# Performance work log

Measured on AMD Instinct MI355X. Metric: run time of the kernel, lower is better.

The kernel has to match this reference:

```python
import jax, jax.numpy as jnp
from jax import lax
import numpy as np

ANCHOR_SCALES = [8, 16, 32]
ANCHOR_RATIOS = [0.5, 1.0, 2.0]
NUM_ANCHOR = len(ANCHOR_SCALES) * len(ANCHOR_RATIOS)
NMS_THRESH = 0.5


def _base_anchors(base_size=16):
    # generate_anchor_in_cell (called with defaults in the torch code)
    a = []
    for s in ANCHOR_SCALES:
        for r in ANCHOR_RATIOS:
            w = base_size * s * np.sqrt(r)
            h = w / r
            xmin = base_size / 2 - w / 2
            ymin = base_size / 2 - h / 2
            a.append([xmin, ymin, xmin + w, ymin + h])
    return np.array(a, dtype=np.float32)  # (A,4)


def _anchors_in_image(H, W, feature_stride):
    base = _base_anchors(16)  # torch code uses default stride for the base cell
    gx = np.arange(0, feature_stride * W, feature_stride)
    gy = np.arange(0, feature_stride * H, feature_stride)
    gx, gy = np.meshgrid(gx, gy)
    grid = np.stack([gx.ravel(), gy.ravel(), gx.ravel(), gy.ravel()], axis=1)  # (K,4)
    anc = (grid[:, None, :] + base[None, :, :]).reshape(-1, 4)  # (K*A,4)
    return jnp.asarray(anc, dtype=jnp.float32)


def _loc2bbox(anchors, loc):
    # anchors: (N,4) xyxy; loc: (B,N,4) (dx,dy,dw,dh)
    w = anchors[:, 2] - anchors[:, 0]
    h = anchors[:, 3] - anchors[:, 1]
    cx = anchors[:, 0] + 0.5 * w
    cy = anchors[:, 1] + 0.5 * h
    dx, dy, dw, dh = loc[..., 0], loc[..., 1], loc[..., 2], loc[..., 3]
    ncx = dx * w + cx
    ncy = dy * h + cy
    nw = jnp.exp(dw) * w
    nh = jnp.exp(dh) * h
    return jnp.stack([ncx - 0.5 * nw, ncy - 0.5 * nh,
                      ncx + 0.5 * nw, ncy + 0.5 * nh], axis=-1)


def _clip_bbox(rois, img_h, img_w):
    x = jnp.clip(rois[..., 0::2], 0.0, img_w)
    y = jnp.clip(rois[..., 1::2], 0.0, img_h)
    out = jnp.stack([x[..., 0], y[..., 0], x[..., 1], y[..., 1]], axis=-1)
    return out


def _nms(boxes, scores, thresh):
    # Greedy NMS. Returns (boxes_sorted_by_score, keep_mask) of fixed shape.
    N = boxes.shape[0]
    order = jnp.argsort(-scores)
    b = boxes[order]
    x1, y1, x2, y2 = b[:, 0], b[:, 1], b[:, 2], b[:, 3]
    areas = (x2 - x1) * (y2 - y1)
    idx = jnp.arange(N)

    def body(i, state):
        suppressed, keep = state
        cur = jnp.logical_not(suppressed[i])
        keep = keep.at[i].set(cur)
        bi = b[i]
        xx1 = jnp.maximum(bi[0], x1)
        yy1 = jnp.maximum(bi[1], y1)
        xx2 = jnp.minimum(bi[2], x2)
        yy2 = jnp.minimum(bi[3], y2)
        inter = jnp.maximum(xx2 - xx1, 0.0) * jnp.maximum(yy2 - yy1, 0.0)
        iou = inter / (areas[i] + areas - inter)
        sup = (iou > thresh) & cur & (idx > i)
        return (suppressed | sup, keep)

    suppressed0 = jnp.zeros((N,), dtype=bool)
    keep0 = jnp.zeros((N,), dtype=bool)
    _, keep = lax.fori_loop(0, N, body, (suppressed0, keep0))
    return b, keep, order


def reference(feature_map, feature_stride, conv_w, conv_b, score_w, score_b, loc_w, loc_b):
    B, C, H, W = feature_map.shape
    anchors = _anchors_in_image(H, W, feature_stride)  # (H*W*A, 4)

    dn = ('NCHW', 'OIHW', 'NCHW')
    mid = jax.nn.relu(lax.conv_general_dilated(
        feature_map, conv_w, (1, 1), ((1, 1), (1, 1)), dimension_numbers=dn)
        + conv_b[None, :, None, None])
    rpn_score = lax.conv_general_dilated(mid, score_w, (1, 1), ((0, 0), (0, 0)),
                                         dimension_numbers=dn) + score_b[None, :, None, None]
    rpn_loc = lax.conv_general_dilated(mid, loc_w, (1, 1), ((0, 0), (0, 0)),
                                       dimension_numbers=dn) + loc_b[None, :, None, None]

    # NCHW -> NHWC -> (B,H,W,A,2), softmax over the 2 classes
    rpn_score = jnp.transpose(rpn_score, (0, 2, 3, 1)).reshape(B, H, W, NUM_ANCHOR, 2)
    rpn_score = jax.nn.softmax(rpn_score, axis=4)
    rpn_loc = jnp.transpose(rpn_loc, (0, 2, 3, 1)).reshape(B, -1, 4)
    rpn_fg_score = rpn_score[..., 1].reshape(B, -1)
    rpn_score = rpn_score.reshape(B, -1, 2)

    rois = _loc2bbox(anchors, rpn_loc)                      # (B,N,4)
    rois = _clip_bbox(rois, H * feature_stride, W * feature_stride)

    # torch code flattens scores across batch -> effectively B == 1
    flat_rois = rois.reshape(-1, 4)
    flat_scores = rpn_fg_score.reshape(-1)
    b_sorted, keep, _ = _nms(lax.stop_gradient(flat_rois),
                             lax.stop_gradient(flat_scores), NMS_THRESH)
    # compacted kept rois (kept first, zero padding) at fixed shape
    order = jnp.argsort(-flat_scores)
    comp = jnp.argsort(~keep)  # stable: kept positions first
    rois_out = (flat_rois[order][comp] * keep[comp][:, None].astype(flat_rois.dtype))

    return rois_out, keep[comp], anchors, rpn_loc, rpn_score


def setup_inputs() -> dict:
    key = jax.random.key(0)
    k1, k2, k3, k4 = jax.random.split(key, 4)
    C_in, C_mid, A = 2048, 256, NUM_ANCHOR
    H, W = 38, 50
    feature_map = jax.random.normal(k1, (1, C_in, H, W), dtype=jnp.float32)
    conv_w = jax.random.normal(k2, (C_mid, C_in, 3, 3), dtype=jnp.float32) * 0.01
    conv_b = jnp.zeros((C_mid,), dtype=jnp.float32)
    score_w = jax.random.normal(k3, (A * 2, C_mid, 1, 1), dtype=jnp.float32) * 0.01
    score_b = jnp.zeros((A * 2,), dtype=jnp.float32)
    loc_w = jax.random.normal(k4, (A * 4, C_mid, 1, 1), dtype=jnp.float32) * 0.01
    loc_b = jnp.zeros((A * 4,), dtype=jnp.float32)
    return {"feature_map": feature_map, "feature_stride": 16,
            "conv_w": conv_w, "conv_b": conv_b,
            "score_w": score_w, "score_b": score_b,
            "loc_w": loc_w, "loc_b": loc_b}
```

## Files before the change

kernel.cpp:

```cpp
#include <hip/hip_runtime.h>
#include <cstdint>

#define U64 unsigned long long

static constexpr int H = 38, W = 50, P = 1900;
static constexpr int CIN = 2048, CMID = 256;
static constexpr int NA = 9, NBOX = 17100;
static constexpr int HP = 40, WP = 52, QP = HP * WP;
static constexpr int TPITCH = 2084;
static constexpr int KS = 7;
static constexpr int NW = 268;
static constexpr int PITCH = 17152;
static constexpr float NMS_T = 0.5f;
static constexpr int QTILE = 256;

static constexpr size_t SZ_INT  = (size_t)CIN * TPITCH * 4;
static constexpr size_t SZ_WT   = (size_t)9 * CIN * CMID * 4;
static constexpr size_t SZ_PART = (size_t)KS * P * CMID * 4;
static constexpr size_t OFF_INT  = 0;
static constexpr size_t OFF_WT   = OFF_INT + SZ_INT;
static constexpr size_t OFF_PART = OFF_WT + SZ_WT;
static constexpr size_t REGA     = OFF_PART + SZ_PART;
static constexpr size_t OFF_MASK = 0;
static constexpr size_t OFF_MID  = REGA;
static constexpr size_t OFF_FG   = OFF_MID + 1945600;
static constexpr size_t OFF_BOX  = OFF_FG + 68608;
static constexpr size_t OFF_SBOX = OFF_BOX + 273664;
static constexpr size_t OFF_SAREA= OFF_SBOX + 273664;
static constexpr size_t OFF_CNT  = OFF_SAREA + 68608;
static constexpr size_t WS_NEED  = OFF_CNT + 68608;

__device__ __forceinline__ U64 rdlane64(U64 v, int l) {
    unsigned lo = (unsigned)__builtin_amdgcn_readlane((int)(unsigned)(v & 0xffffffffull), l);
    unsigned hi = (unsigned)__builtin_amdgcn_readlane((int)(unsigned)(v >> 32), l);
    return ((U64)hi << 32) | (U64)lo;
}


__global__ __launch_bounds__(256) void k_sentinel(float* out, int n) {
    int i = blockIdx.x * 256 + threadIdx.x;
    if (i < n) out[i] = 1.2345678e8f;
}

__global__ __launch_bounds__(256) void k_in_t(const float* __restrict__ fm, float* __restrict__ in_tT) {
    int idx = blockIdx.x * 256 + threadIdx.x;
    if (idx >= CIN * (H * W)) return;
    int ci = idx / (H * W), hw = idx - ci * (H * W);
    int h = hw / W, w = hw - h * W;
    in_tT[(size_t)ci * TPITCH + (h + 1) * WP + 1 + w] = fm[idx];
}

__global__ __launch_bounds__(256) void k_w_t(const float* __restrict__ cw, float* __restrict__ w2) {
    int idx = blockIdx.x * 256 + threadIdx.x;
    if (idx >= CMID * CIN * 9) return;
    int co = idx / (CIN * 9);
    int rem = idx - co * (CIN * 9);
    int ci = rem / 9, k = rem - ci * 9;
    w2[((size_t)(co >> 3) * CIN + ci) * 72 + k * 8 + (co & 7)] = cw[idx];
}

__global__ __launch_bounds__(256, 2) void k_conv(const float* __restrict__ in_tT,
                                                 const float* __restrict__ w2,
                                                 float* __restrict__ partial) {
    __shared__ float4 s_in4[16 * 104];
    int t = threadIdx.x;
    int lane = t & 63;
    int sub = __builtin_amdgcn_readfirstlane(t >> 6);

    int raw = blockIdx.x;
    int xcd = raw & 7, i0 = raw >> 3;
    int L = xcd * 63 + i0;
    int z = L / 72;
    int r0 = L - z * 72;
    int bx = r0 % 9, by = r0 / 9;
    int q0 = bx * QTILE;
    int cout0 = by * 32;
    int cin0 = (z <= 1) ? 304 * z : 608 + 288 * (z - 2);
    int cin1 = cin0 + ((z <= 1) ? 304 : 288);

    float acc[4][8];
#pragma unroll
    for (int j = 0; j < 4; ++j)
#pragma unroll
        for (int c = 0; c < 8; ++c) acc[j][c] = 0.f;

    const float* wbase = w2 + (size_t)(by * 4 + sub) * CIN * 72;

    for (int c0 = cin0; c0 < cin1; c0 += 16) {
        for (int idx = t; idx < 16 * 92; idx += 256) {
            int r = idx / 92, j = idx - r * 92;
            int qf = q0 - 56 + 4 * j;
            float4 v = make_float4(0.f, 0.f, 0.f, 0.f);
            if (qf >= 0 && qf <= 2080)
                v = *reinterpret_cast<const float4*>(in_tT + (size_t)(c0 + r) * TPITCH + qf);
            s_in4[r * 104 + j + (j >> 3)] = v;
        }
        __syncthreads();
#pragma unroll 1
        for (int r = 0; r < 16; ++r) {
            const float4* row4 = s_in4 + r * 104;
            const float4* w4 = reinterpret_cast<const float4*>(wbase + (size_t)(c0 + r) * 72);
#pragma unroll
            for (int dy = 0; dy < 3; ++dy) {
                int v0 = lane + 13 * dy;
                int v1 = v0 + 1, v2 = v0 + 2;
                float4 F0 = row4[v0 + (v0 >> 3)];
                float4 F1 = row4[v1 + (v1 >> 3)];
                float4 F2 = row4[v2 + (v2 >> 3)];
                float F[12] = {F0.x, F0.y, F0.z, F0.w, F1.x, F1.y, F1.z, F1.w,
                               F2.x, F2.y, F2.z, F2.w};
#pragma unroll
                for (int dxi = 0; dxi < 3; ++dxi) {
                    int k = dy * 3 + dxi;
                    float4 wa = w4[k * 2], wb = w4[k * 2 + 1];
                    float wv[8] = {wa.x, wa.y, wa.z, wa.w, wb.x, wb.y, wb.z, wb.w};
#pragma unroll
                    for (int jj = 0; jj < 4; ++jj) {
                        float iv = F[jj + dxi + 3];
#pragma unroll
                        for (int c = 0; c < 8; ++c) acc[jj][c] += iv * wv[c];
                    }
                }
            }
        }
        __syncthreads();
    }
    float* part = partial + (size_t)z * P * CMID;
#pragma unroll
    for (int jj = 0; jj < 4; ++jj) {
        int q = q0 + 4 * lane + jj;
        if (q < QP) {
            int hp = q / WP, wp_ = q - hp * WP;
            if (hp >= 1 && hp <= H && wp_ >= 1 && wp_ <= W) {
                int p = (hp - 1) * W + (wp_ - 1);
                float* dst = part + (size_t)p * CMID + cout0 + sub * 8;
                float4* d4 = reinterpret_cast<float4*>(dst);
                d4[0] = make_float4(acc[jj][0], acc[jj][1], acc[jj][2], acc[jj][3]);
                d4[1] = make_float4(acc[jj][4], acc[jj][5], acc[jj][6], acc[jj][7]);
            }
        }
    }
}

__global__ __launch_bounds__(256) void k_reduce(const float* __restrict__ partial,
                                                const float* __restrict__ bias,
                                                float* __restrict__ mid) {
    int p = blockIdx.x, c = threadIdx.x;
    float s = bias[c];
    for (int ks = 0; ks < KS; ++ks) s += partial[(size_t)ks * P * CMID + (size_t)p * CMID + c];
    mid[(size_t)p * CMID + c] = fmaxf(s, 0.f);
}

__global__ __launch_bounds__(256) void k_heads(const float* __restrict__ mid,
                                               const float* __restrict__ score_w,
                                               const float* __restrict__ score_b,
                                               const float* __restrict__ loc_w,
                                               const float* __restrict__ loc_b,
                                               float* __restrict__ score_out,
                                               float* __restrict__ loc_out,
                                               float* __restrict__ anch_out,
                                               float* __restrict__ fg,
                                               float* __restrict__ boxes) {
    __shared__ float wl[256][56];
    __shared__ float bias[56];
    __shared__ float dots[4][64];
    int t = threadIdx.x;
    for (int idx = t; idx < 18 * 256; idx += 256) {
        int c = idx >> 8, i = idx & 255;
        wl[i][c] = score_w[idx];
    }
    for (int idx = t; idx < 36 * 256; idx += 256) {
        int c = idx >> 8, i = idx & 255;
        wl[i][18 + c] = loc_w[idx];
    }
    if (t < 18) bias[t] = score_b[t];
    else if (t < 54) bias[t] = loc_b[t - 18];
    __syncthreads();

    int pl = t >> 6, c = t & 63;
    for (int rep = 0; rep < 4; ++rep) {
        int p = blockIdx.x * 16 + rep * 4 + pl;
        if (c < 54 && p < P) {
            float d = bias[c];
            const float4* mp = reinterpret_cast<const float4*>(mid + (size_t)p * CMID);
            for (int i4 = 0; i4 < 64; ++i4) {
                float4 m4 = mp[i4];
                int i = i4 * 4;
                d += m4.x * wl[i][c] + m4.y * wl[i + 1][c] + m4.z * wl[i + 2][c] + m4.w * wl[i + 3][c];
            }
            dots[pl][c] = d;
        }
        __syncthreads();
        if (c < NA && p < P) {
            int a = c;
            int idx = p * NA + a;
            float l0 = dots[pl][2 * a], l1 = dots[pl][2 * a + 1];
            float mx = fmaxf(l0, l1);
            float e0 = expf(l0 - mx), e1 = expf(l1 - mx);
            float den = e0 + e1;
            float s0 = e0 / den, s1 = e1 / den;
            score_out[(size_t)idx * 2 + 0] = s0;
            score_out[(size_t)idx * 2 + 1] = s1;
            fg[idx] = s1;
            float dx = dots[pl][18 + 4 * a + 0];
            float dy = dots[pl][18 + 4 * a + 1];
            float dw = dots[pl][18 + 4 * a + 2];
            float dh = dots[pl][18 + 4 * a + 3];
            loc_out[(size_t)idx * 4 + 0] = dx;
            loc_out[(size_t)idx * 4 + 1] = dy;
            loc_out[(size_t)idx * 4 + 2] = dw;
            loc_out[(size_t)idx * 4 + 3] = dh;
            int hh = p / W, ww = p % W;
            const double scales[3] = {8.0, 16.0, 32.0};
            const double ratios[3] = {0.5, 1.0, 2.0};
            double s = scales[a / 3], r = ratios[a % 3];
            double wb2 = 16.0 * s * sqrt(r);
            double hb = wb2 / r;
            double xmin = 8.0 - wb2 / 2.0, ymin = 8.0 - hb / 2.0;
            float b0 = (float)xmin, b1 = (float)ymin;
            float b2 = (float)(xmin + wb2), b3 = (float)(ymin + hb);
            float gx = (float)(ww * 16), gy = (float)(hh * 16);
            float a0 = gx + b0, a1 = gy + b1, a2 = gx + b2, a3 = gy + b3;
            anch_out[(size_t)idx * 4 + 0] = a0;
            anch_out[(size_t)idx * 4 + 1] = a1;
            anch_out[(size_t)idx * 4 + 2] = a2;
            anch_out[(size_t)idx * 4 + 3] = a3;
            float aw = a2 - a0, ah = a3 - a1;
            float cx = a0 + 0.5f * aw, cy = a1 + 0.5f * ah;
            float ncx = dx * aw + cx, ncy = dy * ah + cy;
            float nw = expf(dw) * aw, nh = expf(dh) * ah;
            float x1 = ncx - 0.5f * nw, y1 = ncy - 0.5f * nh;
            float x2 = ncx + 0.5f * nw, y2 = ncy + 0.5f * nh;
            x1 = fminf(fmaxf(x1, 0.f), (float)(W * 16));
            x2 = fminf(fmaxf(x2, 0.f), (float)(W * 16));
            y1 = fminf(fmaxf(y1, 0.f), (float)(H * 16));
            y2 = fminf(fmaxf(y2, 0.f), (float)(H * 16));
            float4* bp = reinterpret_cast<float4*>(boxes);
            bp[idx] = make_float4(x1, y1, x2, y2);
        }
        __syncthreads();
    }
}

static constexpr int JSL = 2144;
__global__ __launch_bounds__(256) void k_rank_part(const float* __restrict__ fg,
                                                   int* __restrict__ cntb) {
    __shared__ float4 tile[256];
    int t = threadIdx.x;
    int i = blockIdx.x * 256 + t;
    int j0 = blockIdx.y * JSL;
    int j1 = min(NBOX, j0 + JSL);
    float my = (i < NBOX) ? fg[i] : 0.f;
    int cnt = 0;
    for (int base = j0; base < j1; base += 1024) {
        int j = base + t * 4;
        float4 v = make_float4(-3.4e38f, -3.4e38f, -3.4e38f, -3.4e38f);
        if (j + 3 < j1) {
            v = *reinterpret_cast<const float4*>(fg + j);
        } else {
            if (j < j1) v.x = fg[j];
            if (j + 1 < j1) v.y = fg[j + 1];
            if (j + 2 < j1) v.z = fg[j + 2];
            if (j + 3 < j1) v.w = fg[j + 3];
        }
        __syncthreads();
        tile[t] = v;
        __syncthreads();
        if (i < NBOX) {
            for (int u = 0; u < 256; ++u) {
                float4 s = tile[u];
                int jb = base + u * 4;
                cnt += (s.x > my) || (s.x == my && jb < i);
                cnt += (s.y > my) || (s.y == my && jb + 1 < i);
                cnt += (s.z > my) || (s.z == my && jb + 2 < i);
                cnt += (s.w > my) || (s.w == my && jb + 3 < i);
            }
        }
    }
    if (i < NBOX && cnt) atomicAdd(&cntb[i], cnt);
}

__global__ __launch_bounds__(256) void k_scatter(const int* __restrict__ cntb,
                                                 const float* __restrict__ boxes,
                                                 float* __restrict__ sboxes,
                                                 float* __restrict__ sarea) {
    int i = blockIdx.x * 256 + threadIdx.x;
    if (i >= NBOX) return;
    int c = cntb[i];
    float4 b = reinterpret_cast<const float4*>(boxes)[i];
    reinterpret_cast<float4*>(sboxes)[c] = b;
    sarea[c] = (b.z - b.x) * (b.w - b.y);
}

__global__ __launch_bounds__(256) void k_maskfill(const float* __restrict__ sboxes,
                                                  const float* __restrict__ sarea,
                                                  U64* __restrict__ maskT) {
    int w = blockIdx.y;
    int i0 = blockIdx.x * 256;
    if (w < (i0 >> 6)) return;
    __shared__ float4 sb[64];
    __shared__ float sa[64];
    int t = threadIdx.x;
    if (t < 64) {
        int j = w * 64 + t;
        if (j < NBOX) {
            sb[t] = reinterpret_cast<const float4*>(sboxes)[j];
            sa[t] = sarea[j];
        } else {
            sb[t] = make_float4(0.f, 0.f, 0.f, 0.f);
            sa[t] = 0.f;
        }
    }
    __syncthreads();
    int i = i0 + t;
    if (i >= NBOX || w < (i >> 6)) return;
    float4 bi = reinterpret_cast<const float4*>(sboxes)[i];
    float ai = sarea[i];
    U64 word = 0;
#pragma unroll 4
    for (int jb = 0; jb < 64; ++jb) {
        int j = w * 64 + jb;
        float4 bj = sb[jb];
        float xx1 = fmaxf(bi.x, bj.x), yy1 = fmaxf(bi.y, bj.y);
        float xx2 = fminf(bi.z, bj.z), yy2 = fminf(bi.w, bj.w);
        float inter = fmaxf(xx2 - xx1, 0.f) * fmaxf(yy2 - yy1, 0.f);
        float iou = inter / (ai + sa[jb] - inter);
        word |= ((U64)((iou > NMS_T) && (j > i))) << jb;
    }
    maskT[(size_t)w * PITCH + i] = word;
}

__global__ __launch_bounds__(256) void k_sweep(const U64* __restrict__ maskT,
                                               const float* __restrict__ sboxes,
                                               float* __restrict__ rois_out,
                                               float* __restrict__ keep_out) {
    __shared__ U64 rem[NW];
    __shared__ U64 diag[2][64];
    __shared__ int klist[64];
    __shared__ unsigned base_s;
    int t = threadIdx.x;
    for (int u = t; u < NW; u += 256) rem[u] = 0;
    if (t == 0) base_s = 0;
    if (t < 64) diag[0][t] = maskT[t];
    __syncthreads();

    for (int g = 0; g < NW; ++g) {
        int nv = min(64, NBOX - g * 64);
        U64 vmask = (nv == 64) ? ~0ull : ((1ull << nv) - 1);

        U64 nxtval = 0;
        if (t < 64 && g + 1 < NW) {
            int row = (g + 1) * 64 + t;
            if (row < NBOX) nxtval = maskT[(size_t)(g + 1) * PITCH + row];
        }

        U64 myw = diag[g & 1][t & 63];
        U64 notsup = ~rem[g] & vmask;
        U64 kept = 0;
        while (notsup) {
            int i = (int)__builtin_ctzll(notsup);
            kept |= (1ull << i);
            U64 wi = rdlane64(myw, i);
            notsup &= ~(wi | (1ull << i));
        }
        int nk = __popcll(kept);
        unsigned base = base_s;

        if (t < 64) {
            if ((kept >> t) & 1ull) {
                unsigned pre = (unsigned)__popcll(kept & ((1ull << t) - 1));
                unsigned dst = base + pre;
                float4 bb = reinterpret_cast<const float4*>(sboxes)[g * 64 + t];
                reinterpret_cast<float4*>(rois_out)[dst] = bb;
                keep_out[dst] = 1.0f;
                klist[pre] = t;
            }
        }
        __syncthreads();

        if (t == 0) base_s = base + (unsigned)nk;

        for (int w = g + 1 + t; w < NW; w += 256) {
            const U64* col = maskT + (size_t)w * PITCH + g * 64;
            U64 acc = rem[w];
            int b = 0;
            for (; b + 7 < nk; b += 8) {
                U64 v0 = col[klist[b]];
                U64 v1 = col[klist[b + 1]];
                U64 v2 = col[klist[b + 2]];
                U64 v3 = col[klist[b + 3]];
                U64 v4 = col[klist[b + 4]];
                U64 v5 = col[klist[b + 5]];
                U64 v6 = col[klist[b + 6]];
                U64 v7 = col[klist[b + 7]];
                acc |= v0 | v1 | v2 | v3 | v4 | v5 | v6 | v7;
            }
            for (; b + 3 < nk; b += 4) {
                U64 v0 = col[klist[b]];
                U64 v1 = col[klist[b + 1]];
                U64 v2 = col[klist[b + 2]];
                U64 v3 = col[klist[b + 3]];
                acc |= v0 | v1 | v2 | v3;
            }
            for (; b < nk; ++b) acc |= col[klist[b]];
            rem[w] = acc;
        }
        if (t < 64) diag[(g + 1) & 1][t] = nxtval;
        __syncthreads();
    }
}

extern "C" void kernel_launch(void* const* d_in, const int* in_sizes, int n_in,
                              void* d_out, int out_size, void* d_ws, size_t ws_size,
                              hipStream_t stream) {
    const float* fm      = (const float*)d_in[0];
    const float* conv_w  = (const float*)d_in[2];
    const float* conv_b  = (const float*)d_in[3];
    const float* score_w = (const float*)d_in[4];
    const float* score_b = (const float*)d_in[5];
    const float* loc_w   = (const float*)d_in[6];
    const float* loc_b   = (const float*)d_in[7];

    float* out = (float*)d_out;
    float* rois_out  = out;
    float* keep_out  = out + NBOX * 4;
    float* anch_out  = out + NBOX * 5;
    float* loc_out   = out + NBOX * 9;
    float* score_out = out + NBOX * 13;

    if (ws_size < WS_NEED) {
        k_sentinel<<<(out_size + 255) / 256, 256, 0, stream>>>(out, out_size);
        return;
    }

    char* ws = (char*)d_ws;
    float* in_tT   = (float*)(ws + OFF_INT);
    float* w2      = (float*)(ws + OFF_WT);
    float* partial = (float*)(ws + OFF_PART);
    U64*   maskT   = (U64*)(ws + OFF_MASK);
    float* mid     = (float*)(ws + OFF_MID);
    float* fg      = (float*)(ws + OFF_FG);
    float* boxes   = (float*)(ws + OFF_BOX);
    float* sboxes  = (float*)(ws + OFF_SBOX);
    float* sarea   = (float*)(ws + OFF_SAREA);
    int*   cntb    = (int*)(ws + OFF_CNT);

    hipMemsetAsync(in_tT, 0, SZ_INT, stream);
    k_in_t<<<(CIN * H * W + 255) / 256, 256, 0, stream>>>(fm, in_tT);
    k_w_t<<<(CMID * CIN * 9 + 255) / 256, 256, 0, stream>>>(conv_w, w2);
    k_conv<<<504, 256, 0, stream>>>(in_tT, w2, partial);
    k_reduce<<<P, 256, 0, stream>>>(partial, conv_b, mid);
    k_heads<<<(P + 15) / 16, 256, 0, stream>>>(mid, score_w, score_b, loc_w, loc_b,
                                               score_out, loc_out, anch_out, fg, boxes);
    hipMemsetAsync(cntb, 0, NBOX * 4, stream);
    k_rank_part<<<dim3((NBOX + 255) / 256, 8), 256, 0, stream>>>(fg, cntb);
    k_scatter<<<(NBOX + 255) / 256, 256, 0, stream>>>(cntb, boxes, sboxes, sarea);
    hipMemsetAsync(rois_out, 0, (size_t)NBOX * 5 * 4, stream);
    k_maskfill<<<dim3((NBOX + 255) / 256, NW), 256, 0, stream>>>(sboxes, sarea, maskT);
    k_sweep<<<1, 256, 0, stream>>>(maskT, sboxes, rois_out, keep_out);
}
```

Baseline: 867.9 us.

## Pipeline NMS sweep: wave0 resolves groups while other waves propagate previous suppression

Restructures the greedy NMS sweep so one wavefront resolves each 64-box group and directly ORs its kept rows into the next group's suppression mask using register-held prefetched words. The remaining three wavefronts propagate the previous group's suppression to later groups one step behind, using atomicOr on shared memory. This halves the block barriers per group and overlaps the serial scan with the column propagation. In exchange it relies on LDS atomics and lagged propagation, and it prefetches mask rows two groups ahead in registers.

New measurement: 852.5 us. No clear change (-1.8%).

```diff
diff --git a/kernel.cpp b/kernel.cpp
--- a/kernel.cpp
+++ b/kernel.cpp
@@ -335,78 +335,91 @@
                                                float* __restrict__ rois_out,
                                                float* __restrict__ keep_out) {
     __shared__ U64 rem[NW];
-    __shared__ U64 diag[2][64];
-    __shared__ int klist[64];
+    __shared__ int klbuf[2][64];
+    __shared__ int kn[2];
     __shared__ unsigned base_s;
     int t = threadIdx.x;
     for (int u = t; u < NW; u += 256) rem[u] = 0;
-    if (t == 0) base_s = 0;
-    if (t < 64) diag[0][t] = maskT[t];
+    if (t == 0) { base_s = 0; kn[0] = 0; kn[1] = 0; }
+
+    U64 dA = 0, nA = 0, dB = 0, nB = 0;
+    if (t < 64) {
+        int r0 = t;
+        dA = maskT[(size_t)0 * PITCH + r0];
+        nA = maskT[(size_t)1 * PITCH + r0];
+        int r1 = 64 + t;
+        dB = maskT[(size_t)1 * PITCH + r1];
+        nB = maskT[(size_t)2 * PITCH + r1];
+    }
     __syncthreads();
 
-    for (int g = 0; g < NW; ++g) {
-        int nv = min(64, NBOX - g * 64);
-        U64 vmask = (nv == 64) ? ~0ull : ((1ull << nv) - 1);
-
-        U64 nxtval = 0;
-        if (t < 64 && g + 1 < NW) {
-            int row = (g + 1) * 64 + t;
-            if (row < NBOX) nxtval = maskT[(size_t)(g + 1) * PITCH + row];
-        }
-
-        U64 myw = diag[g & 1][t & 63];
-        U64 notsup = ~rem[g] & vmask;
-        U64 kept = 0;
-        while (notsup) {
-            int i = (int)__builtin_ctzll(notsup);
-            kept |= (1ull << i);
-            U64 wi = rdlane64(myw, i);
-            notsup &= ~(wi | (1ull << i));
-        }
-        int nk = __popcll(kept);
-        unsigned base = base_s;
-
+    auto body = [&](int g, U64& dR, U64& nR) {
         if (t < 64) {
-            if ((kept >> t) & 1ull) {
+            int nv = min(64, NBOX - g * 64);
+            U64 vmask = (nv == 64) ? ~0ull : ((1ull << nv) - 1);
+            U64 m = rem[g];
+            U64 notsup = ~m & vmask;
+            U64 kept = 0;
+            while (notsup) {
+                int i = (int)__builtin_ctzll(notsup);
+                kept |= (1ull << i);
+                U64 wi = rdlane64(dR, i);
+                notsup &= ~(wi | (1ull << i));
+            }
+            int nk = __popcll(kept);
+            bool mine = (kept >> t) & 1ull;
+
+            U64 val = mine ? nR : 0;
+#pragma unroll
+            for (int s = 1; s < 64; s <<= 1) val |= (U64)__shfl_xor((unsigned long long)val, s, 64);
+            if (t == 0 && g + 1 < NW && val) atomicOr(&rem[g + 1], val);
+
+            if (g + 2 < NW) {
+                int row = (g + 2) * 64 + t;
+                dR = (row < NBOX) ? maskT[(size_t)(g + 2) * PITCH + row] : 0;
+                nR = (row < NBOX && g + 3 < NW) ? maskT[(size_t)(g + 3) * PITCH + row] : 0;
+            }
+
+            unsigned base = base_s;
+            if (mine) {
                 unsigned pre = (unsigned)__popcll(kept & ((1ull << t) - 1));
                 unsigned dst = base + pre;
                 float4 bb = reinterpret_cast<const float4*>(sboxes)[g * 64 + t];
                 reinterpret_cast<float4*>(rois_out)[dst] = bb;
                 keep_out[dst] = 1.0f;
-                klist[pre] = t;
-            }
-        }
-        __syncthreads();
-
-        if (t == 0) base_s = base + (unsigned)nk;
-
-        for (int w = g + 1 + t; w < NW; w += 256) {
-            const U64* col = maskT + (size_t)w * PITCH + g * 64;
-            U64 acc = rem[w];
-            int b = 0;
-            for (; b + 7 < nk; b += 8) {
-                U64 v0 = col[klist[b]];
-                U64 v1 = col[klist[b + 1]];
-                U64 v2 = col[klist[b + 2]];
-                U64 v3 = col[klist[b + 3]];
-                U64 v4 = col[klist[b + 4]];
-                U64 v5 = col[klist[b + 5]];
-                U64 v6 = col[klist[b + 6]];
-                U64 v7 = col[klist[b + 7]];
-                acc |= v0 | v1 | v2 | v3 | v4 | v5 | v6 | v7;
-            }
-            for (; b + 3 < nk; b += 4) {
-                U64 v0 = col[klist[b]];
-                U64 v1 = col[klist[b + 1]];
-                U64 v2 = col[klist[b + 2]];
-                U64 v3 = col[klist[b + 3]];
-                acc |= v0 | v1 | v2 | v3;
-            }
-            for (; b < nk; ++b) acc |= col[klist[b]];
-            rem[w] = acc;
-        }
-        if (t < 64) diag[(g + 1) & 1][t] = nxtval;
-        __syncthreads();
+                klbuf[g & 1][pre] = t;
+            }
+            if (t == 0) {
+                kn[g & 1] = nk;
+                base_s = base + (unsigned)nk;
+            }
+        } else if (g >= 1) {
+            int pb = (g - 1) & 1;
+            int nkp = kn[pb];
+            if (nkp) {
+                const size_t colbase = (size_t)(g - 1) * 64;
+                for (int w = g + 1 + (t - 64); w < NW; w += 192) {
+                    const U64* col = maskT + (size_t)w * PITCH + colbase;
+                    U64 acc = 0;
+                    int b = 0;
+                    for (; b + 3 < nkp; b += 4) {
+                        U64 v0 = col[klbuf[pb][b]];
+                        U64 v1 = col[klbuf[pb][b + 1]];
+                        U64 v2 = col[klbuf[pb][b + 2]];
+                        U64 v3 = col[klbuf[pb][b + 3]];
+                        acc |= v0 | v1 | v2 | v3;
+                    }
+                    for (; b < nkp; ++b) acc |= col[klbuf[pb][b]];
+                    if (acc) atomicOr(&rem[w], acc);
+                }
+            }
+        }
+        __syncthreads();
+    };
+
+    for (int gg = 0; gg < NW; gg += 2) {
+        body(gg, dA, nA);
+        body(gg + 1, dB, nB);
     }
 }
 
```
